# Performance work log

Hardware: AMD Instinct MI355X
Metric: run time of the kernel (lower is better)

## Reference

```python
import jax, jax.numpy as jnp
import numpy as np

# Static graph-batch geometry (equal-size graphs -> uniform per-graph k, jit-friendly)
B = 512        # number of graphs
N_PER = 2048   # nodes per graph
C = 64         # in_channels
DEG = 16       # average degree
K = 1024       # ceil(ratio * N_PER) with ratio = 0.5
N = B * N_PER
E = B * N_PER * DEG


def setup_inputs() -> dict:
    key = jax.random.key(0)
    k1, k2, k3 = jax.random.split(key, 3)
    x = jax.random.normal(k1, (N, C), dtype=jnp.float32)
    # edges are intra-graph: local endpoints in [0, N_PER) plus per-graph node offset
    local = jax.random.randint(k2, (2, E), 0, N_PER, dtype=jnp.int32)
    offs = jnp.repeat(jnp.arange(B, dtype=jnp.int32) * N_PER, N_PER * DEG)
    edge_index = local + offs[None, :]
    batch = jnp.repeat(jnp.arange(B, dtype=jnp.int32), N_PER)
    p = jax.random.normal(k3, (C,), dtype=jnp.float32)  # SelectTopK projection weight
    return {"x": x, "edge_index": edge_index, "batch": batch, "p": p}


def reference(x, edge_index, batch, p):
    # SelectTopK: y = tanh(x @ p / ||p||), per-graph top-k
    y = jnp.tanh(x @ p / jnp.linalg.norm(p))            # [N]
    scores, local_idx = jax.lax.top_k(y.reshape(B, N_PER), K)   # [B, K] each
    perm = (local_idx.astype(jnp.int32)
            + jnp.arange(B, dtype=jnp.int32)[:, None] * N_PER).reshape(-1)  # [B*K] global ids
    score = scores.reshape(-1)                          # [B*K]
    # gather + scale (multiplier == 1)
    x_out = x[perm] * score[:, None]                    # [B*K, C]
    # FilterEdges / connect: remap kept nodes to new contiguous ids, mask dropped edges
    node_map = jnp.full((N,), -1, dtype=jnp.int32).at[perm].set(
        jnp.arange(B * K, dtype=jnp.int32))
    new_src = node_map[edge_index[0]]
    new_dst = node_map[edge_index[1]]
    edge_mask = (new_src >= 0) & (new_dst >= 0)         # [E] which edges survive
    new_edge_index = jnp.where(edge_mask[None, :],
                               jnp.stack([new_src, new_dst]), -1)  # dropped edges = -1
    new_batch = batch[perm]
    return x_out, new_edge_index, new_batch, perm, score
```

## Files before the change

kernel.cpp:

```cpp
#include <hip/hip_runtime.h>
#include <cstdint>
#include <cstddef>

#define NB 512
#define N_PER 2048
#define NC 64
#define DEG 16
#define KSEL 1024
#define NTOT (NB * N_PER)
#define ETOT (NTOT * DEG)
#define NOUT (NB * KSEL)


__global__ __launch_bounds__(256) void score_sort_kernel(
    const float* __restrict__ x, const float* __restrict__ p,
    float* __restrict__ out_batch, float* __restrict__ out_perm,
    float* __restrict__ out_score, int* __restrict__ node_map,
    int* __restrict__ perm_i) {
  __shared__ double y_s[N_PER];
  __shared__ unsigned long long key_s[N_PER];
  __shared__ double p_s[NC];
  __shared__ double norm_s;

  const int tid = threadIdx.x;
  const int b = blockIdx.x;

  if (tid < NC) p_s[tid] = (double)p[tid];
  __syncthreads();
  if (tid == 0) {
    double s = 0.0;
    for (int i = 0; i < NC; ++i) s += p_s[i] * p_s[i];
    norm_s = sqrt(s);
  }
  __syncthreads();
  const double norm = norm_s;

  const int lane = tid & 15;
  const int rowg = tid >> 4;
  const double pw0 = p_s[lane * 4 + 0];
  const double pw1 = p_s[lane * 4 + 1];
  const double pw2 = p_s[lane * 4 + 2];
  const double pw3 = p_s[lane * 4 + 3];
  const float4* xrow = (const float4*)(x + (size_t)b * N_PER * NC);

  for (int r0 = 0; r0 < N_PER; r0 += 16) {
    const int row = r0 + rowg;
    float4 v = xrow[row * 16 + lane];
    double part = (double)v.x * pw0 + (double)v.y * pw1 +
                  (double)v.z * pw2 + (double)v.w * pw3;
    part += __shfl_xor(part, 8, 16);
    part += __shfl_xor(part, 4, 16);
    part += __shfl_xor(part, 2, 16);
    part += __shfl_xor(part, 1, 16);
    if (lane == 0) y_s[row] = tanh(part / norm);
  }
  __syncthreads();

  for (int i = tid; i < N_PER; i += 256) {
    unsigned long long u = (unsigned long long)__double_as_longlong(y_s[i]);
    unsigned long long asc =
        (u & 0x8000000000000000ULL) ? ~u : (u | 0x8000000000000000ULL);
    unsigned long long desc = ~asc;
    key_s[i] = (desc & ~2047ULL) | (unsigned long long)i;
  }
  __syncthreads();

  for (int k = 2; k <= N_PER; k <<= 1) {
    for (int j = k >> 1; j > 0; j >>= 1) {
      for (int t = tid; t < N_PER / 2; t += 256) {
        const int i = 2 * t - (t & (j - 1));
        const int partner = i + j;
        const unsigned long long a = key_s[i];
        const unsigned long long c = key_s[partner];
        const bool up = ((i & k) == 0);
        if ((a > c) == up) {
          key_s[i] = c;
          key_s[partner] = a;
        }
      }
      __syncthreads();
    }
  }

  for (int t = tid; t < N_PER; t += 256) {
    const int idx = (int)(key_s[t] & 2047ULL);
    const int g = b * N_PER + idx;
    if (t < KSEL) {
      const int nid = b * KSEL + t;
      node_map[g] = nid;
      perm_i[nid] = g;
      out_batch[nid] = (float)b;
      out_perm[nid] = (float)g;
      out_score[nid] = (float)y_s[idx];
    } else {
      node_map[g] = -1;
    }
  }
}

__global__ __launch_bounds__(256) void gather_kernel(
    const float* __restrict__ x, const int* __restrict__ perm_i,
    const float* __restrict__ score, float* __restrict__ x_out) {
  const int t = blockIdx.x * 256 + threadIdx.x;
  const int row = t >> 4;
  const int lane = t & 15;
  const int g = perm_i[row];
  const float sc = score[row];
  float4 v = ((const float4*)x)[(size_t)g * 16 + lane];
  v.x *= sc; v.y *= sc; v.z *= sc; v.w *= sc;
  ((float4*)x_out)[(size_t)row * 16 + lane] = v;
}

__global__ __launch_bounds__(256) void edge_kernel(
    const int* __restrict__ ei, const int* __restrict__ node_map,
    float* __restrict__ out_edge) {
  const int i = blockIdx.x * 256 + threadIdx.x;
  const int4 s4 = ((const int4*)ei)[i];
  const int4 d4 = ((const int4*)(ei + (size_t)ETOT))[i];
  const int ns0 = node_map[s4.x], ns1 = node_map[s4.y];
  const int ns2 = node_map[s4.z], ns3 = node_map[s4.w];
  const int nd0 = node_map[d4.x], nd1 = node_map[d4.y];
  const int nd2 = node_map[d4.z], nd3 = node_map[d4.w];
  float4 os, od;
  const bool k0 = (ns0 >= 0) && (nd0 >= 0);
  const bool k1 = (ns1 >= 0) && (nd1 >= 0);
  const bool k2 = (ns2 >= 0) && (nd2 >= 0);
  const bool k3 = (ns3 >= 0) && (nd3 >= 0);
  os.x = k0 ? (float)ns0 : -1.0f; od.x = k0 ? (float)nd0 : -1.0f;
  os.y = k1 ? (float)ns1 : -1.0f; od.y = k1 ? (float)nd1 : -1.0f;
  os.z = k2 ? (float)ns2 : -1.0f; od.z = k2 ? (float)nd2 : -1.0f;
  os.w = k3 ? (float)ns3 : -1.0f; od.w = k3 ? (float)nd3 : -1.0f;
  ((float4*)out_edge)[i] = os;
  ((float4*)(out_edge + (size_t)ETOT))[i] = od;
}

extern "C" void kernel_launch(void* const* d_in, const int* in_sizes, int n_in,
                              void* d_out, int out_size, void* d_ws,
                              size_t ws_size, hipStream_t stream) {
  const float* x = (const float*)d_in[0];
  const int* ei = (const int*)d_in[1];
  const float* p = (const float*)d_in[3];

  float* out = (float*)d_out;
  float* out_x = out;
  float* out_edge = out + 33554432;
  float* out_batch = out + 67108864;
  float* out_perm = out + 67633152;
  float* out_score = out + 68157440;

  int* node_map = (int*)d_ws;
  int* perm_i = node_map + NTOT;

  score_sort_kernel<<<NB, 256, 0, stream>>>(x, p, out_batch, out_perm,
                                            out_score, node_map, perm_i);
  gather_kernel<<<(NOUT * 16) / 256, 256, 0, stream>>>(x, perm_i, out_score,
                                                       out_x);
  edge_kernel<<<(ETOT / 4) / 256, 256, 0, stream>>>(ei, node_map, out_edge);
}
```

Measured before the change: 665.3 us.

## Fuse scoring, register bitonic sort, gather and edge remap into one per-graph kernel

Merges the three kernels into a single per-graph block of 512 threads. The bitonic sort now holds 4 keys per thread in registers and uses wave shuffles for strides inside a wavefront, touching shared memory only for large strides. The node map is kept in shared memory per graph, so the global node_map/perm workspace and its scattered global lookups go away. Sorting now uses the raw dot product instead of the tanh value, and the score is recomputed in float tanhf, which could differ slightly in rounding. The main risk is that only 512 blocks carry the bandwidth-heavy gather and edge work, which may limit memory parallelism.

```diff
diff --git a/kernel.cpp b/kernel.cpp
--- a/kernel.cpp
+++ b/kernel.cpp
@@ -11,19 +11,26 @@
 #define ETOT (NTOT * DEG)
 #define NOUT (NB * KSEL)
 
-
-__global__ __launch_bounds__(256) void score_sort_kernel(
+#define T 512
+#define EPT 4
+
+
+__global__ __launch_bounds__(T) void fused_topk_kernel(
     const float* __restrict__ x, const float* __restrict__ p,
+    const int* __restrict__ ei,
+    float* __restrict__ out_x, float* __restrict__ out_edge,
     float* __restrict__ out_batch, float* __restrict__ out_perm,
-    float* __restrict__ out_score, int* __restrict__ node_map,
-    int* __restrict__ perm_i) {
-  __shared__ double y_s[N_PER];
-  __shared__ unsigned long long key_s[N_PER];
+    float* __restrict__ out_score) {
+  __shared__ unsigned long long key2[EPT][T];
+  __shared__ int lmap[N_PER];
+  __shared__ int klist[KSEL];
+  __shared__ float kscore[KSEL];
   __shared__ double p_s[NC];
   __shared__ double norm_s;
 
   const int tid = threadIdx.x;
   const int b = blockIdx.x;
+  const int base = b * N_PER;
 
   if (tid < NC) p_s[tid] = (double)p[tid];
   __syncthreads();
@@ -32,8 +39,6 @@
     for (int i = 0; i < NC; ++i) s += p_s[i] * p_s[i];
     norm_s = sqrt(s);
   }
-  __syncthreads();
-  const double norm = norm_s;
 
   const int lane = tid & 15;
   const int rowg = tid >> 4;
@@ -41,9 +46,9 @@
   const double pw1 = p_s[lane * 4 + 1];
   const double pw2 = p_s[lane * 4 + 2];
   const double pw3 = p_s[lane * 4 + 3];
-  const float4* xrow = (const float4*)(x + (size_t)b * N_PER * NC);
-
-  for (int r0 = 0; r0 < N_PER; r0 += 16) {
+  const float4* xrow = (const float4*)(x + (size_t)base * NC);
+
+  for (int r0 = 0; r0 < N_PER; r0 += 32) {
     const int row = r0 + rowg;
     float4 v = xrow[row * 16 + lane];
     double part = (double)v.x * pw0 + (double)v.y * pw1 +
@@ -52,86 +57,129 @@
     part += __shfl_xor(part, 4, 16);
     part += __shfl_xor(part, 2, 16);
     part += __shfl_xor(part, 1, 16);
-    if (lane == 0) y_s[row] = tanh(part / norm);
-  }
-  __syncthreads();
-
-  for (int i = tid; i < N_PER; i += 256) {
-    unsigned long long u = (unsigned long long)__double_as_longlong(y_s[i]);
-    unsigned long long asc =
-        (u & 0x8000000000000000ULL) ? ~u : (u | 0x8000000000000000ULL);
-    unsigned long long desc = ~asc;
-    key_s[i] = (desc & ~2047ULL) | (unsigned long long)i;
-  }
-  __syncthreads();
-
-  for (int k = 2; k <= N_PER; k <<= 1) {
-    for (int j = k >> 1; j > 0; j >>= 1) {
-      for (int t = tid; t < N_PER / 2; t += 256) {
-        const int i = 2 * t - (t & (j - 1));
-        const int partner = i + j;
-        const unsigned long long a = key_s[i];
-        const unsigned long long c = key_s[partner];
-        const bool up = ((i & k) == 0);
-        if ((a > c) == up) {
-          key_s[i] = c;
-          key_s[partner] = a;
-        }
-      }
-      __syncthreads();
-    }
-  }
-
-  for (int t = tid; t < N_PER; t += 256) {
-    const int idx = (int)(key_s[t] & 2047ULL);
-    const int g = b * N_PER + idx;
-    if (t < KSEL) {
-      const int nid = b * KSEL + t;
-      node_map[g] = nid;
-      perm_i[nid] = g;
+    if (lane == 0) {
+      unsigned long long u = (unsigned long long)__double_as_longlong(part);
+      unsigned long long asc =
+          (u & 0x8000000000000000ULL) ? ~u : (u | 0x8000000000000000ULL);
+      unsigned long long desc = ~asc;
+      key2[row & 3][row >> 2] = (desc & ~2047ULL) | (unsigned long long)row;
+    }
+  }
+  __syncthreads();
+
+  unsigned long long r[EPT];
+#pragma unroll
+  for (int s = 0; s < EPT; ++s) r[s] = key2[s][tid];
+
+  auto CE = [](unsigned long long& a, unsigned long long& c, bool up) {
+    if ((a > c) == up) { unsigned long long t = a; a = c; c = t; }
+  };
+  auto shfl_stage = [&](int m, bool up) {
+    const bool keepmin = (((tid & m) == 0) == up);
+#pragma unroll
+    for (int s = 0; s < EPT; ++s) {
+      unsigned long long o = __shfl_xor(r[s], m, 64);
+      const bool take = keepmin ? (o < r[s]) : (o > r[s]);
+      if (take) r[s] = o;
+    }
+  };
+  auto lds_stage = [&](int m, bool up) {
+    __syncthreads();
+#pragma unroll
+    for (int s = 0; s < EPT; ++s) key2[s][tid] = r[s];
+    __syncthreads();
+    const bool keepmin = (((tid & m) == 0) == up);
+#pragma unroll
+    for (int s = 0; s < EPT; ++s) {
+      unsigned long long o = key2[s][tid ^ m];
+      const bool take = keepmin ? (o < r[s]) : (o > r[s]);
+      if (take) r[s] = o;
+    }
+  };
+
+  CE(r[0], r[1], true);
+  CE(r[2], r[3], false);
+  {
+    const bool up = ((tid & 1) == 0);
+    CE(r[0], r[2], up); CE(r[1], r[3], up);
+    CE(r[0], r[1], up); CE(r[2], r[3], up);
+  }
+#pragma unroll
+  for (int k = 8; k <= N_PER; k <<= 1) {
+    const bool up = ((tid & (k >> 2)) == 0);
+#pragma unroll
+    for (int j = (k >> 1); j >= 256; j >>= 1) lds_stage(j >> 2, up);
+#pragma unroll
+    for (int j = ((k >> 1) > 128 ? 128 : (k >> 1)); j >= 4; j >>= 1)
+      shfl_stage(j >> 2, up);
+    CE(r[0], r[2], up); CE(r[1], r[3], up);
+    CE(r[0], r[1], up); CE(r[2], r[3], up);
+  }
+
+  __syncthreads();
+  const double norm = norm_s;
+#pragma unroll
+  for (int s = 0; s < EPT; ++s) {
+    const int pos = tid * EPT + s;
+    const int idx = (int)(r[s] & 2047ULL);
+    if (pos < KSEL) {
+      unsigned long long desc = r[s] & ~2047ULL;
+      unsigned long long asc = ~desc;
+      unsigned long long u = (asc & 0x8000000000000000ULL)
+                                 ? (asc ^ 0x8000000000000000ULL)
+                                 : ~asc;
+      const double dot = __longlong_as_double((long long)u);
+      const float sc = tanhf((float)(dot / norm));
+      const int nid = b * KSEL + pos;
       out_batch[nid] = (float)b;
-      out_perm[nid] = (float)g;
-      out_score[nid] = (float)y_s[idx];
+      out_perm[nid] = (float)(base + idx);
+      out_score[nid] = sc;
+      klist[pos] = idx;
+      kscore[pos] = sc;
+      lmap[idx] = nid;
     } else {
-      node_map[g] = -1;
-    }
-  }
-}
-
-__global__ __launch_bounds__(256) void gather_kernel(
-    const float* __restrict__ x, const int* __restrict__ perm_i,
-    const float* __restrict__ score, float* __restrict__ x_out) {
-  const int t = blockIdx.x * 256 + threadIdx.x;
-  const int row = t >> 4;
-  const int lane = t & 15;
-  const int g = perm_i[row];
-  const float sc = score[row];
-  float4 v = ((const float4*)x)[(size_t)g * 16 + lane];
-  v.x *= sc; v.y *= sc; v.z *= sc; v.w *= sc;
-  ((float4*)x_out)[(size_t)row * 16 + lane] = v;
-}
-
-__global__ __launch_bounds__(256) void edge_kernel(
-    const int* __restrict__ ei, const int* __restrict__ node_map,
-    float* __restrict__ out_edge) {
-  const int i = blockIdx.x * 256 + threadIdx.x;
-  const int4 s4 = ((const int4*)ei)[i];
-  const int4 d4 = ((const int4*)(ei + (size_t)ETOT))[i];
-  const int ns0 = node_map[s4.x], ns1 = node_map[s4.y];
-  const int ns2 = node_map[s4.z], ns3 = node_map[s4.w];
-  const int nd0 = node_map[d4.x], nd1 = node_map[d4.y];
-  const int nd2 = node_map[d4.z], nd3 = node_map[d4.w];
-  float4 os, od;
-  const bool k0 = (ns0 >= 0) && (nd0 >= 0);
-  const bool k1 = (ns1 >= 0) && (nd1 >= 0);
-  const bool k2 = (ns2 >= 0) && (nd2 >= 0);
-  const bool k3 = (ns3 >= 0) && (nd3 >= 0);
-  os.x = k0 ? (float)ns0 : -1.0f; od.x = k0 ? (float)nd0 : -1.0f;
-  os.y = k1 ? (float)ns1 : -1.0f; od.y = k1 ? (float)nd1 : -1.0f;
-  os.z = k2 ? (float)ns2 : -1.0f; od.z = k2 ? (float)nd2 : -1.0f;
-  os.w = k3 ? (float)ns3 : -1.0f; od.w = k3 ? (float)nd3 : -1.0f;
-  ((float4*)out_edge)[i] = os;
-  ((float4*)(out_edge + (size_t)ETOT))[i] = od;
+      lmap[idx] = -1;
+    }
+  }
+  __syncthreads();
+
+  const float4* xg = (const float4*)x;
+  float4* xo = (float4*)out_x;
+#pragma unroll 4
+  for (int rr = 0; rr < KSEL; rr += 32) {
+    const int row = rr + rowg;
+    const int idx = klist[row];
+    const float sc = kscore[row];
+    float4 v = xg[(size_t)(base + idx) * 16 + lane];
+    v.x *= sc; v.y *= sc; v.z *= sc; v.w *= sc;
+    xo[(size_t)(b * KSEL + row) * 16 + lane] = v;
+  }
+
+  const int nE4 = N_PER * DEG / 4;
+  const int4* s_ei = (const int4*)ei + (size_t)b * nE4;
+  const int4* d_ei = (const int4*)(ei + (size_t)ETOT) + (size_t)b * nE4;
+  float4* o_s = (float4*)out_edge + (size_t)b * nE4;
+  float4* o_d = (float4*)(out_edge + (size_t)ETOT) + (size_t)b * nE4;
+#pragma unroll 2
+  for (int i = tid; i < nE4; i += T) {
+    const int4 s4 = s_ei[i];
+    const int4 d4 = d_ei[i];
+    const int ns0 = lmap[s4.x - base], ns1 = lmap[s4.y - base];
+    const int ns2 = lmap[s4.z - base], ns3 = lmap[s4.w - base];
+    const int nd0 = lmap[d4.x - base], nd1 = lmap[d4.y - base];
+    const int nd2 = lmap[d4.z - base], nd3 = lmap[d4.w - base];
+    float4 os, od;
+    const bool k0 = (ns0 >= 0) && (nd0 >= 0);
+    const bool k1 = (ns1 >= 0) && (nd1 >= 0);
+    const bool k2 = (ns2 >= 0) && (nd2 >= 0);
+    const bool k3 = (ns3 >= 0) && (nd3 >= 0);
+    os.x = k0 ? (float)ns0 : -1.0f; od.x = k0 ? (float)nd0 : -1.0f;
+    os.y = k1 ? (float)ns1 : -1.0f; od.y = k1 ? (float)nd1 : -1.0f;
+    os.z = k2 ? (float)ns2 : -1.0f; od.z = k2 ? (float)nd2 : -1.0f;
+    os.w = k3 ? (float)ns3 : -1.0f; od.w = k3 ? (float)nd3 : -1.0f;
+    o_s[i] = os;
+    o_d[i] = od;
+  }
 }
 
 extern "C" void kernel_launch(void* const* d_in, const int* in_sizes, int n_in,
@@ -148,12 +196,6 @@
   float* out_perm = out + 67633152;
   float* out_score = out + 68157440;
 
-  int* node_map = (int*)d_ws;
-  int* perm_i = node_map + NTOT;
-
-  score_sort_kernel<<<NB, 256, 0, stream>>>(x, p, out_batch, out_perm,
-                                            out_score, node_map, perm_i);
-  gather_kernel<<<(NOUT * 16) / 256, 256, 0, stream>>>(x, perm_i, out_score,
-                                                       out_x);
-  edge_kernel<<<(ETOT / 4) / 256, 256, 0, stream>>>(ei, node_map, out_edge);
+  fused_topk_kernel<<<NB, T, 0, stream>>>(x, p, ei, out_x, out_edge, out_batch,
+                                          out_perm, out_score);
 }
```

Measured after the change: 572.4 us. -14.0%, faster.
